# Kernel tuning notes

Measured on AMD Instinct MI355X. Metric: run time of the kernel, lower is better.

## Reference

```python
import jax, jax.numpy as jnp
import numpy as np
from functools import partial

TAU = 2.0
V_TH = 1.0
ALPHA = 2.0  # spikingjelly surrogate.ATan default alpha
EPS = 1e-5   # nn.LayerNorm default eps

@jax.custom_vjp
def atan_spike(v):
    # Heaviside forward; ATan surrogate gradient in bwd.
    return (v >= 0.0).astype(v.dtype)

def _atan_fwd(v):
    return atan_spike(v), v

def _atan_bwd(v, g):
    sg = (ALPHA / 2.0) / (1.0 + (jnp.pi / 2.0 * ALPHA * v) ** 2)
    return (g * sg,)

atan_spike.defvjp(_atan_fwd, _atan_bwd)

def lif_multi_step(x):
    # x: [B, T, H]; LIF with decay_input=True, v_reset=0 (hard reset), detach_reset=True.
    xt = jnp.swapaxes(x, 0, 1)  # [T, B, H]
    v0 = jnp.zeros(x.shape[:1] + x.shape[2:], dtype=x.dtype)  # reset_net per call
    def step(v, x_t):
        v = v + (x_t - v) / TAU            # charge
        s = atan_spike(v - V_TH)           # fire (surrogate grad)
        v = v * (1.0 - jax.lax.stop_gradient(s))  # hard reset to 0, detached spike
        return v, s
    _, spikes = jax.lax.scan(step, v0, xt)
    return jnp.swapaxes(spikes, 0, 1)  # [B, T, H]

def layer_norm(x, gamma, beta):
    mu = jnp.mean(x, axis=-1, keepdims=True)
    var = jnp.mean((x - mu) ** 2, axis=-1, keepdims=True)
    return (x - mu) * jax.lax.rsqrt(var + EPS) * gamma + beta

def setup_inputs() -> dict:
    key = jax.random.key(0)
    ks = jax.random.split(key, 5)
    B, T, D, H = 64, 1024, 256, 512
    x = jax.random.normal(ks[0], (B, T, D), dtype=jnp.float32)
    sc1 = 1.0 / np.sqrt(D)
    sc2 = 1.0 / np.sqrt(H)
    W1 = jax.random.uniform(ks[1], (H, D), jnp.float32, -sc1, sc1)
    b1 = jax.random.uniform(ks[2], (H,), jnp.float32, -sc1, sc1)
    W2 = jax.random.uniform(ks[3], (D, H), jnp.float32, -sc2, sc2)
    b2 = jax.random.uniform(ks[4], (D,), jnp.float32, -sc2, sc2)
    g1 = jnp.ones((H,), jnp.float32); be1 = jnp.zeros((H,), jnp.float32)
    g2 = jnp.ones((D,), jnp.float32); be2 = jnp.zeros((D,), jnp.float32)
    return {"x": x, "W1": W1, "b1": b1, "g1": g1, "be1": be1,
            "W2": W2, "b2": b2, "g2": g2, "be2": be2}

def reference(x, W1, b1, g1, be1, W2, b2, g2, be2):
    residual = x
    h = jnp.einsum('btd,hd->bth', x, W1) + b1   # fc1
    h = layer_norm(h, g1, be1)                   # norm1
    h = lif_multi_step(h)                        # lif1 (dropout = identity, eval)
    y = jnp.einsum('bth,dh->btd', h, W2) + b2    # fc2
    y = layer_norm(y, g2, be2)                   # norm2
    y = lif_multi_step(y)                        # lif2
    return residual + y
```

## Files before the change

### kernel.cpp

```cpp
#include <hip/hip_runtime.h>

typedef int   v4i __attribute__((ext_vector_type(4)));
typedef int  v16i __attribute__((ext_vector_type(16)));
typedef float v4f __attribute__((ext_vector_type(4)));

#define TT 1024
#define DD 256
#define HH 512
#define CB 32
#define CM (CB*TT)

static __device__ __forceinline__ double shfl_xor_d(double x, int m) {
    union { double d; int u[2]; } a; a.d = x;
    a.u[0] = __shfl_xor(a.u[0], m);
    a.u[1] = __shfl_xor(a.u[1], m);
    return a.d;
}

__global__ __launch_bounds__(256) void prep_w_k(const float* __restrict__ W1,
                                                const float* __restrict__ W2,
                                                signed char* __restrict__ W1p,
                                                signed char* __restrict__ W2p) {
    int i = blockIdx.x * 256 + threadIdx.x;
    {
        double a = (double)W1[i];
        double inv = 1024.0, s = 1.0 / 1024.0;
#pragma unroll
        for (int p = 0; p < 5; ++p) {
            int d = (int)(a * inv);
            a -= d * s;
            W1p[(size_t)p * 131072 + i] = (signed char)d;
            inv *= 128.0; s *= (1.0 / 128.0);
        }
    }
    {
        double a = (double)W2[i];
        double inv = 1024.0, s = 1.0 / 1024.0;
#pragma unroll
        for (int p = 0; p < 5; ++p) {
            int d = (int)(a * inv);
            a -= d * s;
            W2p[(size_t)p * 131072 + i] = (signed char)d;
            inv *= 128.0; s *= (1.0 / 128.0);
        }
    }
}

__global__ __launch_bounds__(256) void split_x_k(const float* __restrict__ xc,
                                                 signed char* __restrict__ Xp) {
    int gid = blockIdx.x * 256 + threadIdx.x;
    int e0 = gid * 4;
    v4f xv = *(const v4f*)(xc + e0);
    int dg[4][5];
#pragma unroll
    for (int e = 0; e < 4; ++e) {
        float a = xv[e];
        float inv = 8.0f, s = 0.125f;
#pragma unroll
        for (int p = 0; p < 5; ++p) {
            int d = (int)(a * inv);
            a -= (float)d * s;
            dg[e][p] = d;
            inv *= 128.0f; s *= (1.0f / 128.0f);
        }
    }
#pragma unroll
    for (int p = 0; p < 5; ++p) {
        int pk = (dg[0][p] & 255) | ((dg[1][p] & 255) << 8) |
                 ((dg[2][p] & 255) << 16) | ((dg[3][p] & 255) << 24);
        *(int*)(Xp + (size_t)p * ((size_t)CM * 256) + e0) = pk;
    }
}

__global__ __launch_bounds__(512, 2) void gemm1_i8(
    const signed char* __restrict__ Xp, const signed char* __restrict__ W1p,
    const float* __restrict__ b1, double* __restrict__ Hn,
    double* __restrict__ PS1w, double* __restrict__ PQ1w) {
    __shared__ signed char Asm[5 * 16384];

    const int tid = threadIdx.x;
    const int wave = tid >> 6, lane = tid & 63, lrow = lane & 31, lhalf = lane >> 5;
    const int wm = wave >> 2, wn = wave & 3;
    const int ch = blockIdx.x;
    const int m0 = blockIdx.y * 64;

    {
        const int r = tid >> 3, k0 = (tid & 7) * 32;
        const int swz = (r & 15) << 4;
#pragma unroll
        for (int p = 0; p < 5; ++p) {
            const signed char* sp = Xp + (size_t)p * ((size_t)CM * 256) +
                                    (size_t)(m0 + r) * 256 + k0;
            v4i v0 = *(const v4i*)(sp);
            v4i v1 = *(const v4i*)(sp + 16);
            *(v4i*)&Asm[p * 16384 + r * 256 + (k0 ^ swz)] = v0;
            *(v4i*)&Asm[p * 16384 + r * 256 + ((k0 + 16) ^ swz)] = v1;
        }
    }

    const int colbase = ch * 256 + wn * 32 + lrow;
    const signed char* bptr = W1p + (size_t)colbase * 256 + lhalf * 16;

    v16i acc[5];
    v4i cbf[5];
#pragma unroll
    for (int j = 0; j < 5; ++j)
        cbf[j] = *(const v4i*)(bptr + (size_t)j * 131072);

    __syncthreads();

    const double scl[5] = {0x1p-13, 0x1p-20, 0x1p-27, 0x1p-34, 0x1p-41};
    const int arow = wm * 32 + lrow;
    const int aswz = (arow & 15) << 4;

#pragma unroll
    for (int p = 0; p < 2; ++p) {
#pragma unroll
        for (int g = 0; g < 5; ++g)
#pragma unroll
            for (int r = 0; r < 16; ++r) acc[g][r] = 0;
#pragma unroll
        for (int ksl = 0; ksl < 8; ++ksl) {
            v4i nbf[5];
            const int s = p * 8 + ksl;
            if (s < 15) {
                const int np = (ksl == 7) ? p + 1 : p;
                const int nk = (ksl == 7) ? 0 : ksl + 1;
#pragma unroll
                for (int j = 0; j < 5; ++j)
                    nbf[j] = *(const v4i*)(bptr + (size_t)j * 131072 + np * 32768 + nk * 32);
            }
            v4i af[5];
#pragma unroll
            for (int i = 0; i < 5; ++i)
                af[i] = *(const v4i*)&Asm[i * 16384 + arow * 256 +
                                          ((ksl * 32 + lhalf * 16) ^ aswz)];
#pragma unroll
            for (int j = 0; j < 5; ++j)
#pragma unroll
                for (int i = 0; i + j < 5; ++i)
                    acc[i + j] = __builtin_amdgcn_mfma_i32_32x32x32_i8(
                        af[i], cbf[j], acc[i + j], 0, 0, 0);
#pragma unroll
            for (int j = 0; j < 5; ++j) cbf[j] = nbf[j];
        }
        const int col = colbase + p * 128;
        const double bcol = (double)b1[col];
        const size_t qbase = (size_t)((ch * 2 + p) * 4 + wn) * CM + m0 + wm * 32;
#pragma unroll
        for (int r = 0; r < 16; ++r) {
            double t = 0.0;
#pragma unroll
            for (int g = 0; g < 5; ++g) t = fma((double)acc[g][r], scl[g], t);
            const double hr = t + bcol;
            const int crow = (r & 3) + 8 * (r >> 2) + 4 * lhalf;
            Hn[(size_t)(m0 + wm * 32 + crow) * HH + col] = hr;
            double ps = hr, pq = hr * hr;
#pragma unroll
            for (int m = 1; m < 32; m <<= 1) {
                ps += shfl_xor_d(ps, m);
                pq += shfl_xor_d(pq, m);
            }
            if (lrow == 0) {
                PS1w[qbase + crow] = ps;
                PQ1w[qbase + crow] = pq;
            }
        }
    }
}

__global__ __launch_bounds__(256) void stats1_fin(const double* __restrict__ PS1w,
                                                  const double* __restrict__ PQ1w,
                                                  double2* __restrict__ MUIV1) {
    int row = blockIdx.x * 256 + threadIdx.x;
    double S = 0.0, Q = 0.0;
#pragma unroll
    for (int q = 0; q < 16; ++q) {
        S += PS1w[(size_t)q * CM + row];
        Q += PQ1w[(size_t)q * CM + row];
    }
    double mu = S * (1.0 / 512.0);
    double var = Q * (1.0 / 512.0) - mu * mu;
    MUIV1[row] = make_double2(mu, 1.0 / sqrt(var + 1e-5));
}

__global__ __launch_bounds__(64) void lif1_k(const double* __restrict__ Hn,
                                             const double2* __restrict__ MUIV,
                                             const float* __restrict__ g1,
                                             const float* __restrict__ be1,
                                             signed char* __restrict__ S) {
    const int b = blockIdx.x >> 3;
    const int h = (blockIdx.x & 7) * 64 + threadIdx.x;
    __shared__ double2 MI[4][16];
    const double* src = Hn + (size_t)b * TT * HH + h;
    signed char* dst = S + (size_t)b * TT * HH + h;
    const double gg = (double)g1[h], be = (double)be1[h];
    if (threadIdx.x < 48)
        MI[threadIdx.x >> 4][threadIdx.x & 15] = MUIV[(size_t)b * TT + threadIdx.x];
    double buf[4][16];
#pragma unroll
    for (int gq = 0; gq < 3; ++gq)
#pragma unroll
        for (int t = 0; t < 16; ++t)
            buf[gq][t] = src[(size_t)(gq * 16 + t) * HH];
    __syncthreads();
    double v = 0.0;
    for (int g4 = 0; g4 < 64; g4 += 4) {
#pragma unroll
        for (int u = 0; u < 4; ++u) {
            const int g = g4 + u;
            __syncthreads();
            if (g + 3 < 64) {
                if (threadIdx.x < 16)
                    MI[(g + 3) & 3][threadIdx.x] =
                        MUIV[(size_t)b * TT + (g + 3) * 16 + threadIdx.x];
#pragma unroll
                for (int t = 0; t < 16; ++t)
                    buf[(u + 3) & 3][t] = src[(size_t)((g + 3) * 16 + t) * HH];
            }
#pragma unroll
            for (int t = 0; t < 16; ++t) {
                const double2 mi = MI[g & 3][t];
                const double x = (buf[u][t] - mi.x) * mi.y * gg + be;
                v += (x - v) * 0.5;
                const bool sp = (v >= 1.0);
                dst[(size_t)(g * 16 + t) * HH] = sp ? 1 : 0;
                if (sp) v = 0.0;
            }
        }
    }
}

__global__ __launch_bounds__(512, 2) void gemm2_i8(
    const signed char* __restrict__ Sb, const signed char* __restrict__ W2p,
    const float* __restrict__ b2, double* __restrict__ Yn,
    double2* __restrict__ MUIV2) {
    __shared__ signed char Asm[64 * 512];
    __shared__ double RSs[8][64], RQs[8][64];

    const int tid = threadIdx.x;
    const int wave = tid >> 6, lane = tid & 63, lrow = lane & 31, lhalf = lane >> 5;
    const int m0 = blockIdx.x * 64;

    {
        const int r = tid >> 3, k0 = (tid & 7) * 64;
        const signed char* sp = Sb + (size_t)(m0 + r) * HH + k0;
        const int swz = (r & 15) << 4;
#pragma unroll
        for (int q = 0; q < 4; ++q) {
            v4i v = *(const v4i*)(sp + q * 16);
            *(v4i*)&Asm[r * 512 + ((k0 + q * 16) ^ swz)] = v;
        }
    }

    const int col = wave * 32 + lrow;
    const signed char* bptr = W2p + (size_t)col * 512 + lhalf * 16;

    v16i acc[5];
    v4i cbf[5];
#pragma unroll
    for (int j = 0; j < 5; ++j) cbf[j] = *(const v4i*)(bptr + (size_t)j * 131072);

    __syncthreads();

    const double scl[5] = {0x1p-10, 0x1p-17, 0x1p-24, 0x1p-31, 0x1p-38};
#pragma unroll
    for (int p = 0; p < 2; ++p) {
#pragma unroll
        for (int g = 0; g < 5; ++g)
#pragma unroll
            for (int r = 0; r < 16; ++r) acc[g][r] = 0;
        const int arow = p * 32 + lrow;
        const int aswz = (arow & 15) << 4;
#pragma unroll
        for (int ksl = 0; ksl < 16; ++ksl) {
            v4i nbf[5];
            const int s = p * 16 + ksl;
            if (s < 31) {
                const int nk = (ksl == 15) ? 0 : ksl + 1;
#pragma unroll
                for (int j = 0; j < 5; ++j)
                    nbf[j] = *(const v4i*)(bptr + (size_t)j * 131072 + nk * 32);
            }
            v4i a = *(const v4i*)&Asm[arow * 512 + ((ksl * 32 + lhalf * 16) ^ aswz)];
#pragma unroll
            for (int j = 0; j < 5; ++j)
                acc[j] = __builtin_amdgcn_mfma_i32_32x32x32_i8(a, cbf[j], acc[j], 0, 0, 0);
#pragma unroll
            for (int j = 0; j < 5; ++j) cbf[j] = nbf[j];
        }
        const double bcol = (double)b2[col];
#pragma unroll
        for (int r = 0; r < 16; ++r) {
            double t = 0.0;
#pragma unroll
            for (int g = 0; g < 5; ++g) t = fma((double)acc[g][r], scl[g], t);
            const double yr = t + bcol;
            const int crow = (r & 3) + 8 * (r >> 2) + 4 * lhalf;
            Yn[(size_t)(m0 + p * 32 + crow) * DD + col] = yr;
            double ps = yr, pq = yr * yr;
#pragma unroll
            for (int m = 1; m < 32; m <<= 1) {
                ps += shfl_xor_d(ps, m);
                pq += shfl_xor_d(pq, m);
            }
            if (lrow == 0) {
                RSs[wave][p * 32 + crow] = ps;
                RQs[wave][p * 32 + crow] = pq;
            }
        }
    }
    __syncthreads();
    if (tid < 64) {
        double Ssum = 0.0, Qsum = 0.0;
#pragma unroll
        for (int w = 0; w < 8; ++w) { Ssum += RSs[w][tid]; Qsum += RQs[w][tid]; }
        const double mu = Ssum * (1.0 / 256.0);
        const double var = Qsum * (1.0 / 256.0) - mu * mu;
        MUIV2[m0 + tid] = make_double2(mu, 1.0 / sqrt(var + 1e-5));
    }
}

__global__ __launch_bounds__(64) void lif2_k(const double* __restrict__ Yn,
                                             const double2* __restrict__ MUIV,
                                             const float* __restrict__ g2,
                                             const float* __restrict__ be2,
                                             const float* __restrict__ X,
                                             float* __restrict__ out) {
    const int b = blockIdx.x >> 2;
    const int d = (blockIdx.x & 3) * 64 + threadIdx.x;
    __shared__ double2 MI[4][16];
    const double* src = Yn + (size_t)b * TT * DD + d;
    const float* xs = X + (size_t)b * TT * DD + d;
    float* dst = out + (size_t)b * TT * DD + d;
    const double gg = (double)g2[d], be = (double)be2[d];
    if (threadIdx.x < 48)
        MI[threadIdx.x >> 4][threadIdx.x & 15] = MUIV[(size_t)b * TT + threadIdx.x];
    double bufy[4][16];
    float bufx[4][16];
#pragma unroll
    for (int gq = 0; gq < 3; ++gq)
#pragma unroll
        for (int t = 0; t < 16; ++t) {
            bufy[gq][t] = src[(size_t)(gq * 16 + t) * DD];
            bufx[gq][t] = xs[(size_t)(gq * 16 + t) * DD];
        }
    __syncthreads();
    double v = 0.0;
    for (int g4 = 0; g4 < 64; g4 += 4) {
#pragma unroll
        for (int u = 0; u < 4; ++u) {
            const int g = g4 + u;
            __syncthreads();
            if (g + 3 < 64) {
                if (threadIdx.x < 16)
                    MI[(g + 3) & 3][threadIdx.x] =
                        MUIV[(size_t)b * TT + (g + 3) * 16 + threadIdx.x];
#pragma unroll
                for (int t = 0; t < 16; ++t) {
                    bufy[(u + 3) & 3][t] = src[(size_t)((g + 3) * 16 + t) * DD];
                    bufx[(u + 3) & 3][t] = xs[(size_t)((g + 3) * 16 + t) * DD];
                }
            }
#pragma unroll
            for (int t = 0; t < 16; ++t) {
                const double2 mi = MI[g & 3][t];
                const double x = (bufy[u][t] - mi.x) * mi.y * gg + be;
                v += (x - v) * 0.5;
                const bool sp = (v >= 1.0);
                __builtin_nontemporal_store(bufx[u][t] + (sp ? 1.0f : 0.0f),
                                            &dst[(size_t)(g * 16 + t) * DD]);
                if (sp) v = 0.0;
            }
        }
    }
}

extern "C" void kernel_launch(void* const* d_in, const int* in_sizes, int n_in,
                              void* d_out, int out_size, void* d_ws, size_t ws_size,
                              hipStream_t stream) {
    const float* x   = (const float*)d_in[0];
    const float* W1  = (const float*)d_in[1];
    const float* b1  = (const float*)d_in[2];
    const float* g1  = (const float*)d_in[3];
    const float* be1 = (const float*)d_in[4];
    const float* W2  = (const float*)d_in[5];
    const float* b2  = (const float*)d_in[6];
    const float* g2  = (const float*)d_in[7];
    const float* be2 = (const float*)d_in[8];
    float* out = (float*)d_out;

    char* ws = (char*)d_ws;
    signed char* W1p = (signed char*)ws;
    signed char* W2p = (signed char*)(ws + (1ull << 20));
    double*      Hn  = (double*)(ws + (2ull << 20));
    signed char* Sb  = (signed char*)(ws + (130ull << 20));
    double*      Yn  = (double*)(ws + (146ull << 20));
    signed char* Xp    = (signed char*)(ws + (146ull << 20));
    double*      PS1w  = (double*)(ws + (186ull << 20));
    double*      PQ1w  = (double*)(ws + (190ull << 20));
    double2*     MUIV1 = (double2*)(ws + (194ull << 20));
    double2*     MUIV2 = (double2*)(ws + (210ull << 20));

    prep_w_k<<<dim3(512), dim3(256), 0, stream>>>(W1, W2, W1p, W2p);

    for (int c = 0; c < 2; ++c) {
        const float* xc = x + (size_t)c * CM * DD;
        float* outc = out + (size_t)c * CM * DD;
        split_x_k<<<dim3(8192), dim3(256), 0, stream>>>(xc, Xp);
        gemm1_i8<<<dim3(2, CM / 64), dim3(512), 0, stream>>>(Xp, W1p, b1, Hn, PS1w, PQ1w);
        stats1_fin<<<dim3(CM / 256), dim3(256), 0, stream>>>(PS1w, PQ1w, MUIV1);
        lif1_k<<<dim3(CB * 8), dim3(64), 0, stream>>>(Hn, MUIV1, g1, be1, Sb);
        gemm2_i8<<<dim3(CM / 64), dim3(512), 0, stream>>>(Sb, W2p, b2, Yn, MUIV2);
        lif2_k<<<dim3(CB * 4), dim3(64), 0, stream>>>(Yn, MUIV2, g2, be2, xc, outc);
    }
}
```

Before: 780.1 us.

## Halve GEMM row tiles to 32 with 256-thread blocks and triple-buffer B prefetch

Both int8 split-precision GEMM kernels now use 32-row M tiles with 4 waves per block instead of 64 rows with 8 waves, doubling the grid and halving shared memory per block. Each wave now covers the full 32 rows of the tile rather than one of two row groups. B-fragment register prefetch goes from double to triple buffering (two k-slices ahead) to hide global load latency better. The aim is more blocks for occupancy and scheduling balance. The cost is that each W fragment loaded from global memory is reused across fewer rows, and the deeper prefetch raises register pressure.

After: 715.2 us. -8.3%, faster.

```diff
diff --git a/kernel.cpp b/kernel.cpp
--- a/kernel.cpp
+++ b/kernel.cpp
@@ -72,17 +72,16 @@
     }
 }
 
-__global__ __launch_bounds__(512, 2) void gemm1_i8(
+__global__ __launch_bounds__(256, 2) void gemm1_i8(
     const signed char* __restrict__ Xp, const signed char* __restrict__ W1p,
     const float* __restrict__ b1, double* __restrict__ Hn,
     double* __restrict__ PS1w, double* __restrict__ PQ1w) {
-    __shared__ signed char Asm[5 * 16384];
+    __shared__ signed char Asm[5 * 8192];
 
     const int tid = threadIdx.x;
-    const int wave = tid >> 6, lane = tid & 63, lrow = lane & 31, lhalf = lane >> 5;
-    const int wm = wave >> 2, wn = wave & 3;
+    const int wn = tid >> 6, lane = tid & 63, lrow = lane & 31, lhalf = lane >> 5;
     const int ch = blockIdx.x;
-    const int m0 = blockIdx.y * 64;
+    const int m0 = blockIdx.y * 32;
 
     {
         const int r = tid >> 3, k0 = (tid & 7) * 32;
@@ -93,25 +92,28 @@
                                     (size_t)(m0 + r) * 256 + k0;
             v4i v0 = *(const v4i*)(sp);
             v4i v1 = *(const v4i*)(sp + 16);
-            *(v4i*)&Asm[p * 16384 + r * 256 + (k0 ^ swz)] = v0;
-            *(v4i*)&Asm[p * 16384 + r * 256 + ((k0 + 16) ^ swz)] = v1;
+            *(v4i*)&Asm[p * 8192 + r * 256 + (k0 ^ swz)] = v0;
+            *(v4i*)&Asm[p * 8192 + r * 256 + ((k0 + 16) ^ swz)] = v1;
         }
     }
 
     const int colbase = ch * 256 + wn * 32 + lrow;
     const signed char* bptr = W1p + (size_t)colbase * 256 + lhalf * 16;
 
+    v4i bf[3][5];
+#pragma unroll
+    for (int s = 0; s < 2; ++s)
+#pragma unroll
+        for (int j = 0; j < 5; ++j)
+            bf[s][j] = *(const v4i*)(bptr + (size_t)j * 131072 +
+                                     (s >> 3) * 32768 + (s & 7) * 32);
+
     v16i acc[5];
-    v4i cbf[5];
-#pragma unroll
-    for (int j = 0; j < 5; ++j)
-        cbf[j] = *(const v4i*)(bptr + (size_t)j * 131072);
 
     __syncthreads();
 
     const double scl[5] = {0x1p-13, 0x1p-20, 0x1p-27, 0x1p-34, 0x1p-41};
-    const int arow = wm * 32 + lrow;
-    const int aswz = (arow & 15) << 4;
+    const int aswz = (lrow & 15) << 4;
 
 #pragma unroll
     for (int p = 0; p < 2; ++p) {
@@ -121,32 +123,29 @@
             for (int r = 0; r < 16; ++r) acc[g][r] = 0;
 #pragma unroll
         for (int ksl = 0; ksl < 8; ++ksl) {
-            v4i nbf[5];
             const int s = p * 8 + ksl;
-            if (s < 15) {
-                const int np = (ksl == 7) ? p + 1 : p;
-                const int nk = (ksl == 7) ? 0 : ksl + 1;
+            if (s + 2 < 16) {
+                const int s2 = s + 2;
 #pragma unroll
                 for (int j = 0; j < 5; ++j)
-                    nbf[j] = *(const v4i*)(bptr + (size_t)j * 131072 + np * 32768 + nk * 32);
+                    bf[s2 % 3][j] = *(const v4i*)(bptr + (size_t)j * 131072 +
+                                                  (s2 >> 3) * 32768 + (s2 & 7) * 32);
             }
             v4i af[5];
 #pragma unroll
             for (int i = 0; i < 5; ++i)
-                af[i] = *(const v4i*)&Asm[i * 16384 + arow * 256 +
+                af[i] = *(const v4i*)&Asm[i * 8192 + lrow * 256 +
                                           ((ksl * 32 + lhalf * 16) ^ aswz)];
 #pragma unroll
             for (int j = 0; j < 5; ++j)
 #pragma unroll
                 for (int i = 0; i + j < 5; ++i)
                     acc[i + j] = __builtin_amdgcn_mfma_i32_32x32x32_i8(
-                        af[i], cbf[j], acc[i + j], 0, 0, 0);
-#pragma unroll
-            for (int j = 0; j < 5; ++j) cbf[j] = nbf[j];
+                        af[i], bf[s % 3][j], acc[i + j], 0, 0, 0);
         }
         const int col = colbase + p * 128;
         const double bcol = (double)b1[col];
-        const size_t qbase = (size_t)((ch * 2 + p) * 4 + wn) * CM + m0 + wm * 32;
+        const size_t qbase = (size_t)((ch * 2 + p) * 4 + wn) * CM + m0;
 #pragma unroll
         for (int r = 0; r < 16; ++r) {
             double t = 0.0;
@@ -154,7 +153,7 @@
             for (int g = 0; g < 5; ++g) t = fma((double)acc[g][r], scl[g], t);
             const double hr = t + bcol;
             const int crow = (r & 3) + 8 * (r >> 2) + 4 * lhalf;
-            Hn[(size_t)(m0 + wm * 32 + crow) * HH + col] = hr;
+            Hn[(size_t)(m0 + crow) * HH + col] = hr;
             double ps = hr, pq = hr * hr;
 #pragma unroll
             for (int m = 1; m < 32; m <<= 1) {
@@ -231,16 +230,16 @@
     }
 }
 
-__global__ __launch_bounds__(512, 2) void gemm2_i8(
+__global__ __launch_bounds__(256, 2) void gemm2_i8(
     const signed char* __restrict__ Sb, const signed char* __restrict__ W2p,
     const float* __restrict__ b2, double* __restrict__ Yn,
     double2* __restrict__ MUIV2) {
-    __shared__ signed char Asm[64 * 512];
-    __shared__ double RSs[8][64], RQs[8][64];
+    __shared__ signed char Asm[32 * 512];
+    __shared__ double RSs[2][4][32], RQs[2][4][32];
 
     const int tid = threadIdx.x;
-    const int wave = tid >> 6, lane = tid & 63, lrow = lane & 31, lhalf = lane >> 5;
-    const int m0 = blockIdx.x * 64;
+    const int wn = tid >> 6, lane = tid & 63, lrow = lane & 31, lhalf = lane >> 5;
+    const int m0 = blockIdx.x * 32;
 
     {
         const int r = tid >> 3, k0 = (tid & 7) * 64;
@@ -253,42 +252,45 @@
         }
     }
 
-    const int col = wave * 32 + lrow;
-    const signed char* bptr = W2p + (size_t)col * 512 + lhalf * 16;
+    const signed char* bptr = W2p + (size_t)(wn * 32 + lrow) * 512 + lhalf * 16;
+
+    v4i bf[3][5];
+#pragma unroll
+    for (int s = 0; s < 2; ++s)
+#pragma unroll
+        for (int j = 0; j < 5; ++j)
+            bf[s][j] = *(const v4i*)(bptr + (size_t)j * 131072 +
+                                     (s >> 4) * 65536 + (s & 15) * 32);
 
     v16i acc[5];
-    v4i cbf[5];
-#pragma unroll
-    for (int j = 0; j < 5; ++j) cbf[j] = *(const v4i*)(bptr + (size_t)j * 131072);
 
     __syncthreads();
 
     const double scl[5] = {0x1p-10, 0x1p-17, 0x1p-24, 0x1p-31, 0x1p-38};
+    const int aswz = (lrow & 15) << 4;
+
 #pragma unroll
     for (int p = 0; p < 2; ++p) {
 #pragma unroll
         for (int g = 0; g < 5; ++g)
 #pragma unroll
             for (int r = 0; r < 16; ++r) acc[g][r] = 0;
-        const int arow = p * 32 + lrow;
-        const int aswz = (arow & 15) << 4;
 #pragma unroll
         for (int ksl = 0; ksl < 16; ++ksl) {
-            v4i nbf[5];
             const int s = p * 16 + ksl;
-            if (s < 31) {
-                const int nk = (ksl == 15) ? 0 : ksl + 1;
+            if (s + 2 < 32) {
+                const int s2 = s + 2;
 #pragma unroll
                 for (int j = 0; j < 5; ++j)
-                    nbf[j] = *(const v4i*)(bptr + (size_t)j * 131072 + nk * 32);
-            }
-            v4i a = *(const v4i*)&Asm[arow * 512 + ((ksl * 32 + lhalf * 16) ^ aswz)];
+                    bf[s2 % 3][j] = *(const v4i*)(bptr + (size_t)j * 131072 +
+                                                  (s2 >> 4) * 65536 + (s2 & 15) * 32);
+            }
+            v4i a = *(const v4i*)&Asm[lrow * 512 + ((ksl * 32 + lhalf * 16) ^ aswz)];
 #pragma unroll
             for (int j = 0; j < 5; ++j)
-                acc[j] = __builtin_amdgcn_mfma_i32_32x32x32_i8(a, cbf[j], acc[j], 0, 0, 0);
-#pragma unroll
-            for (int j = 0; j < 5; ++j) cbf[j] = nbf[j];
-        }
+                acc[j] = __builtin_amdgcn_mfma_i32_32x32x32_i8(a, bf[s % 3][j], acc[j], 0, 0, 0);
+        }
+        const int col = p * 128 + wn * 32 + lrow;
         const double bcol = (double)b2[col];
 #pragma unroll
         for (int r = 0; r < 16; ++r) {
@@ -297,7 +299,7 @@
             for (int g = 0; g < 5; ++g) t = fma((double)acc[g][r], scl[g], t);
             const double yr = t + bcol;
             const int crow = (r & 3) + 8 * (r >> 2) + 4 * lhalf;
-            Yn[(size_t)(m0 + p * 32 + crow) * DD + col] = yr;
+            Yn[(size_t)(m0 + crow) * DD + col] = yr;
             double ps = yr, pq = yr * yr;
 #pragma unroll
             for (int m = 1; m < 32; m <<= 1) {
@@ -305,16 +307,18 @@
                 pq += shfl_xor_d(pq, m);
             }
             if (lrow == 0) {
-                RSs[wave][p * 32 + crow] = ps;
-                RQs[wave][p * 32 + crow] = pq;
+                RSs[p][wn][crow] = ps;
+                RQs[p][wn][crow] = pq;
             }
         }
     }
     __syncthreads();
-    if (tid < 64) {
+    if (tid < 32) {
         double Ssum = 0.0, Qsum = 0.0;
 #pragma unroll
-        for (int w = 0; w < 8; ++w) { Ssum += RSs[w][tid]; Qsum += RQs[w][tid]; }
+        for (int p = 0; p < 2; ++p)
+#pragma unroll
+            for (int w = 0; w < 4; ++w) { Ssum += RSs[p][w][tid]; Qsum += RQs[p][w][tid]; }
         const double mu = Ssum * (1.0 / 256.0);
         const double var = Qsum * (1.0 / 256.0) - mu * mu;
         MUIV2[m0 + tid] = make_double2(mu, 1.0 / sqrt(var + 1e-5));
@@ -408,10 +412,10 @@
         const float* xc = x + (size_t)c * CM * DD;
         float* outc = out + (size_t)c * CM * DD;
         split_x_k<<<dim3(8192), dim3(256), 0, stream>>>(xc, Xp);
-        gemm1_i8<<<dim3(2, CM / 64), dim3(512), 0, stream>>>(Xp, W1p, b1, Hn, PS1w, PQ1w);
+        gemm1_i8<<<dim3(2, CM / 32), dim3(256), 0, stream>>>(Xp, W1p, b1, Hn, PS1w, PQ1w);
         stats1_fin<<<dim3(CM / 256), dim3(256), 0, stream>>>(PS1w, PQ1w, MUIV1);
         lif1_k<<<dim3(CB * 8), dim3(64), 0, stream>>>(Hn, MUIV1, g1, be1, Sb);
-        gemm2_i8<<<dim3(CM / 64), dim3(512), 0, stream>>>(Sb, W2p, b2, Yn, MUIV2);
+        gemm2_i8<<<dim3(CM / 32), dim3(256), 0, stream>>>(Sb, W2p, b2, Yn, MUIV2);
         lif2_k<<<dim3(CB * 4), dim3(64), 0, stream>>>(Yn, MUIV2, g2, be2, xc, outc);
     }
 }
```
